# Kernel optimization log

Measured on AMD Instinct MI355X. Metric: run time of the kernel, lower is better.

Reference implementation:

```python
import jax, jax.numpy as jnp
import numpy as np

HIDDEN = 512
N_CLASSES = 10

def setup_inputs() -> dict:
    key = jax.random.key(0)
    ks = jax.random.split(key, 7)
    B, T, H = 256, 784, HIDDEN
    s_ih = 1.0 / np.sqrt(H)
    inputs = jax.random.normal(ks[0], (B, T), dtype=jnp.float32)
    # nn.LSTMCell(1, H) parameters, gate order i, f, g, o
    W_ih = jax.random.uniform(ks[1], (4 * H, 1), jnp.float32, -s_ih, s_ih)
    W_hh = jax.random.uniform(ks[2], (4 * H, H), jnp.float32, -s_ih, s_ih)
    b_ih = jax.random.uniform(ks[3], (4 * H,), jnp.float32, -s_ih, s_ih)
    b_hh = jax.random.uniform(ks[4], (4 * H,), jnp.float32, -s_ih, s_ih)
    # nn.Linear(H, 10)
    W_lin = jax.random.uniform(ks[5], (N_CLASSES, H), jnp.float32, -s_ih, s_ih)
    b_lin = jax.random.uniform(ks[6], (N_CLASSES,), jnp.float32, -s_ih, s_ih)
    return {"inputs": inputs, "W_ih": W_ih, "W_hh": W_hh, "b_ih": b_ih,
            "b_hh": b_hh, "W_lin": W_lin, "b_lin": b_lin}

def reference(inputs, W_ih, W_hh, b_ih, b_hh, W_lin, b_lin):
    B = inputs.shape[0]
    H = W_hh.shape[1]
    w_in = W_ih[:, 0]          # [4H], input feature dim is 1
    bias = b_ih + b_hh         # [4H]

    def step(carry, x_t):
        h, c = carry
        # gates: [B, 4H] = x contribution + recurrent matmul + bias
        gates = x_t[:, None] * w_in[None, :] + h @ W_hh.T + bias
        i, f, g, o = jnp.split(gates, 4, axis=1)
        c_new = jax.nn.sigmoid(f) * c + jax.nn.sigmoid(i) * jnp.tanh(g)
        h_new = jax.nn.sigmoid(o) * jnp.tanh(c_new)
        return (h_new, c_new), None

    h0 = jnp.zeros((B, H), dtype=inputs.dtype)
    c0 = jnp.zeros((B, H), dtype=inputs.dtype)
    (h_T, _), _ = jax.lax.scan(step, (h0, c0), inputs.T)  # scan over T
    return h_T @ W_lin.T + b_lin  # [B, n_classes]
```

## Files before the change

kernel.cpp:

```cpp
#include <hip/hip_runtime.h>
#include <hip/hip_bf16.h>
#include <cmath>

#define HID 512
#define TSTEPS 784
#define BATCH 256
#define NCLS 10
#define NBLK 256
#define NGRP 16

typedef __bf16 bf16x8 __attribute__((ext_vector_type(8)));
typedef float f32x4 __attribute__((ext_vector_type(4)));
typedef float f32x2 __attribute__((ext_vector_type(2)));
typedef int   i32x4 __attribute__((ext_vector_type(4)));

#define SWS(r) (((unsigned)(r) & 7u) << 4)

#define LDX4_CC(dst, addr) \
    asm volatile("global_load_dwordx4 %0, %1, off sc0 sc1" : "=v"(dst) : "v"(addr) : "memory")
#define STOREDW_CC(addr, val) \
    asm volatile("global_store_dword %0, %1, off sc0 sc1" :: "v"(addr), "v"(val) : "memory")

__device__ __forceinline__ unsigned lddw_cc_wait(const unsigned* a) {
    unsigned d;
    asm volatile("global_load_dword %0, %1, off sc0 sc1\n\ts_waitcnt vmcnt(0)"
                 : "=v"(d) : "v"(a) : "memory");
    return d;
}

__global__ void init_all(const float* __restrict__ x, float* __restrict__ xT,
                         uint4* __restrict__ hz, unsigned* __restrict__ flg) {
    int t = blockIdx.x, tid = threadIdx.x;
    xT[t * BATCH + tid] = x[tid * TSTEPS + t];
    int i = t * 256 + tid;
    if (i < (512 << 10) / 16) hz[i] = make_uint4(0u, 0u, 0u, 0u);
    if (i < NGRP * 64) flg[i] = 0u;
}

__device__ __forceinline__ float sigmoid_f(float v) {
    return __fdividef(1.f, 1.f + __expf(-v));
}
__device__ __forceinline__ float tanh_f(float v) {
    float e = __expf(fminf(fmaxf(2.f * v, -30.f), 30.f));
    return __fdividef(e - 1.f, e + 1.f);
}

__global__ __launch_bounds__(512)
void lstm_persist(const float* __restrict__ xT,
                  const float* __restrict__ W_hh,
                  const float* __restrict__ w_in,
                  const float* __restrict__ b_ih,
                  const float* __restrict__ b_hh,
                  __bf16* __restrict__ h0,
                  __bf16* __restrict__ h1,
                  float* __restrict__ hf,
                  unsigned* __restrict__ flg)
{
    __shared__ __align__(16) __bf16 wlds[128 * HID];
    __shared__ __align__(16) __bf16 hlds[16 * HID];
    __shared__ float gl[4][16][33];
    __shared__ float xl[16];

    const int tid  = threadIdx.x;
    const int lane = tid & 63;
    const int w    = tid >> 6;
    const int s    = w & 3;
    const int ch   = w >> 2;
    const int bg   = blockIdx.x >> 4;
    const int cs   = blockIdx.x & 15;
    const int b0   = bg * 16;
    const int j0   = cs * 32;
    const int rlo  = lane & 15;
    const int khi  = (lane >> 4) * 8;

    unsigned* flags = flg + bg * 64;

    {
        int r = tid >> 2;
        int q = tid & 3;
        int gs = r >> 5, jj = r & 31;
        const float* src = W_hh + (size_t)(gs * HID + j0 + jj) * HID + q * 128;
        char* wp = (char*)wlds;
        unsigned rowb = (unsigned)r * (HID * 2);
        unsigned sw   = SWS(r);
        #pragma unroll
        for (int cc = 0; cc < 128; cc += 8) {
            float4 va = *(const float4*)(src + cc);
            float4 vb = *(const float4*)(src + cc + 4);
            bf16x8 pk;
            pk[0]=(__bf16)va.x; pk[1]=(__bf16)va.y; pk[2]=(__bf16)va.z; pk[3]=(__bf16)va.w;
            pk[4]=(__bf16)vb.x; pk[5]=(__bf16)vb.y; pk[6]=(__bf16)vb.z; pk[7]=(__bf16)vb.w;
            *(bf16x8*)(wp + ((rowb + (unsigned)(q * 128 + cc) * 2) ^ sw)) = pk;
        }
    }

    float win_l, bias_l;
    {
        int idx = s * HID + j0 + ch * 16 + rlo;
        win_l  = w_in[idx];
        bias_l = b_ih[idx] + b_hh[idx];
    }

    const int Rc  = tid >> 5;
    const int col = tid & 31;
    float creg = 0.f;

    const int rS  = tid >> 5;
    const int seg = tid & 31;
    const unsigned rowbS = (unsigned)rS * (HID * 2);
    const unsigned swS   = SWS(rS);
    const unsigned* myflag = flags + (seg >> 1);

    const unsigned rBb = (unsigned)(s * 32 + ch * 16 + rlo) * (HID * 2);
    const unsigned swB = SWS(rlo);
    const char* wbp = (const char*)wlds;
    const char* hbp = (const char*)hlds;
    char* hwp = (char*)hlds;

    __syncthreads();

    for (int t = 0; t < TSTEPS; ++t) {
        const __bf16* hprev = (t & 1) ? h1 : h0;
        __bf16* hnext       = (t & 1) ? h0 : h1;

        if (tid < 16) xl[tid] = xT[t * BATCH + b0 + tid];
        {
            while (lddw_cc_wait(myflag) < (unsigned)t) __builtin_amdgcn_s_sleep(1);
            const __bf16* gsrc = hprev + (size_t)(b0 + rS) * HID + seg * 16;
            i32x4 v0, v1;
            LDX4_CC(v0, gsrc);
            LDX4_CC(v1, gsrc + 8);
            asm volatile("s_waitcnt vmcnt(0)" ::: "memory");
            __builtin_amdgcn_sched_barrier(0);
            unsigned base = rowbS + (unsigned)seg * 32u;
            *(i32x4*)(hwp + ((base +  0u) ^ swS)) = v0;
            *(i32x4*)(hwp + ((base + 16u) ^ swS)) = v1;
        }
        __syncthreads();

        f32x4 acc_e, acc_o = {0.f,0.f,0.f,0.f};
        #pragma unroll
        for (int rr = 0; rr < 4; ++rr)
            acc_e[rr] = xl[(lane >> 4) * 4 + rr] * win_l + bias_l;
        #pragma unroll
        for (int ks = 0; ks < 16; ks += 2) {
            unsigned colb0 = (unsigned)(khi * 2 + ks * 64);
            unsigned colb1 = colb0 + 64u;
            bf16x8 a0 = *(const bf16x8*)(hbp + (((unsigned)rlo * 1024u + colb0) ^ SWS(rlo)));
            bf16x8 b0f = *(const bf16x8*)(wbp + ((rBb + colb0) ^ swB));
            bf16x8 a1 = *(const bf16x8*)(hbp + (((unsigned)rlo * 1024u + colb1) ^ SWS(rlo)));
            bf16x8 b1f = *(const bf16x8*)(wbp + ((rBb + colb1) ^ swB));
            acc_e = __builtin_amdgcn_mfma_f32_16x16x32_bf16(a0, b0f, acc_e, 0, 0, 0);
            acc_o = __builtin_amdgcn_mfma_f32_16x16x32_bf16(a1, b1f, acc_o, 0, 0, 0);
        }
        f32x4 acc0 = acc_e + acc_o;
        #pragma unroll
        for (int rr = 0; rr < 4; ++rr) {
            int rowl = (lane >> 4) * 4 + rr;
            gl[s][rowl][ch * 16 + rlo] = acc0[rr];
        }
        __syncthreads();

        {
            float gi = gl[0][Rc][col];
            float gf = gl[1][Rc][col];
            float gg = gl[2][Rc][col];
            float go = gl[3][Rc][col];
            float cn = sigmoid_f(gf) * creg + sigmoid_f(gi) * tanh_f(gg);
            creg = cn;
            float hn = sigmoid_f(go) * tanh_f(cn);
            float hn_o = __shfl_xor(hn, 1);
            if (t == TSTEPS - 1) {
                if (!(tid & 1))
                    *(f32x2*)(hf + (size_t)(b0 + Rc) * HID + j0 + col) = (f32x2){hn, hn_o};
            } else {
                if (!(tid & 1)) {
                    union { __bf16 b[2]; int i; } u;
                    u.b[0] = (__bf16)hn; u.b[1] = (__bf16)hn_o;
                    __bf16* dst = hnext + (size_t)(b0 + Rc) * HID + j0 + col;
                    STOREDW_CC(dst, u.i);
                }
            }
        }
        if (t == TSTEPS - 1) break;

        asm volatile("s_waitcnt vmcnt(0)" ::: "memory");
        __syncthreads();
        if (tid == 0) STOREDW_CC(flags + cs, (int)(t + 1));
    }
}

__global__ void head(const float* __restrict__ hfp, const float* __restrict__ Wl,
                     const float* __restrict__ bl_, float* __restrict__ out)
{
    __shared__ float hr[HID];
    int b = blockIdx.x;
    for (int k = threadIdx.x; k < HID; k += blockDim.x) hr[k] = hfp[b * HID + k];
    __syncthreads();
    int j = threadIdx.x;
    if (j < NCLS) {
        float acc = bl_[j];
        for (int k = 0; k < HID; ++k) acc += hr[k] * Wl[j * HID + k];
        out[b * NCLS + j] = acc;
    }
}

extern "C" void kernel_launch(void* const* d_in, const int* in_sizes, int n_in,
                              void* d_out, int out_size, void* d_ws, size_t ws_size,
                              hipStream_t stream) {
    const float* inputs = (const float*)d_in[0];
    const float* W_ih   = (const float*)d_in[1];
    const float* W_hh   = (const float*)d_in[2];
    const float* b_ih   = (const float*)d_in[3];
    const float* b_hh   = (const float*)d_in[4];
    const float* W_lin  = (const float*)d_in[5];
    const float* b_lin  = (const float*)d_in[6];

    const size_t OFS_H1  = 256u << 10;
    const size_t OFS_HF  = 512u << 10;
    const size_t OFS_XT  = 1024u << 10;
    const size_t OFS_FLG = OFS_XT + (size_t)TSTEPS * BATCH * 4;
    const size_t NEEDED  = OFS_FLG + NGRP * 64 * 4;
    if (ws_size < NEEDED) return;

    char* ws = (char*)d_ws;
    __bf16* h0 = (__bf16*)ws;
    __bf16* h1 = (__bf16*)(ws + OFS_H1);
    float*  hf = (float*)(ws + OFS_HF);
    float*  xT = (float*)(ws + OFS_XT);
    unsigned* flg = (unsigned*)(ws + OFS_FLG);

    init_all<<<TSTEPS, BATCH, 0, stream>>>(inputs, xT, (uint4*)h0, flg);

    lstm_persist<<<NBLK, 512, 0, stream>>>(xT, W_hh, W_ih, b_ih, b_hh,
                                           h0, h1, hf, flg);

    head<<<BATCH, 64, 0, stream>>>(hf, W_lin, b_lin, (float*)d_out);
}
```

Measured before the change: 2.698 ms.

## Interleave gate rows in LDS weights so each wave computes full LSTM cells via shuffles

Reorders the bf16 W_hh rows in shared memory so that the four gates (i,f,g,o) of each hidden unit sit in adjacent MFMA output columns within one wave. The cell update then runs on the MFMA accumulators directly using lane shuffles, which removes the gate staging array in LDS and one block-wide barrier per timestep. In exchange, every lane evaluates all four gate nonlinearities redundantly across the 4-lane group, and the h stores become narrower and more scattered.

```diff
diff --git a/kernel.cpp b/kernel.cpp
--- a/kernel.cpp
+++ b/kernel.cpp
@@ -58,14 +58,11 @@
 {
     __shared__ __align__(16) __bf16 wlds[128 * HID];
     __shared__ __align__(16) __bf16 hlds[16 * HID];
-    __shared__ float gl[4][16][33];
     __shared__ float xl[16];
 
     const int tid  = threadIdx.x;
     const int lane = tid & 63;
     const int w    = tid >> 6;
-    const int s    = w & 3;
-    const int ch   = w >> 2;
     const int bg   = blockIdx.x >> 4;
     const int cs   = blockIdx.x & 15;
     const int b0   = bg * 16;
@@ -78,8 +75,9 @@
     {
         int r = tid >> 2;
         int q = tid & 3;
-        int gs = r >> 5, jj = r & 31;
-        const float* src = W_hh + (size_t)(gs * HID + j0 + jj) * HID + q * 128;
+        int wv = r >> 4, tc = r & 15;
+        int g = tc & 3, jj = tc >> 2;
+        const float* src = W_hh + (size_t)(g * HID + j0 + wv * 4 + jj) * HID + q * 128;
         char* wp = (char*)wlds;
         unsigned rowb = (unsigned)r * (HID * 2);
         unsigned sw   = SWS(r);
@@ -94,16 +92,15 @@
         }
     }
 
+    const int g_l  = rlo & 3;
+    const int jj_l = rlo >> 2;
     float win_l, bias_l;
     {
-        int idx = s * HID + j0 + ch * 16 + rlo;
+        int idx = g_l * HID + j0 + w * 4 + jj_l;
         win_l  = w_in[idx];
         bias_l = b_ih[idx] + b_hh[idx];
     }
-
-    const int Rc  = tid >> 5;
-    const int col = tid & 31;
-    float creg = 0.f;
+    float creg4[4] = {0.f, 0.f, 0.f, 0.f};
 
     const int rS  = tid >> 5;
     const int seg = tid & 31;
@@ -111,7 +108,7 @@
     const unsigned swS   = SWS(rS);
     const unsigned* myflag = flags + (seg >> 1);
 
-    const unsigned rBb = (unsigned)(s * 32 + ch * 16 + rlo) * (HID * 2);
+    const unsigned rBb = (unsigned)(w * 16 + rlo) * (HID * 2);
     const unsigned swB = SWS(rlo);
     const char* wbp = (const char*)wlds;
     const char* hbp = (const char*)hlds;
@@ -153,32 +150,28 @@
             acc_e = __builtin_amdgcn_mfma_f32_16x16x32_bf16(a0, b0f, acc_e, 0, 0, 0);
             acc_o = __builtin_amdgcn_mfma_f32_16x16x32_bf16(a1, b1f, acc_o, 0, 0, 0);
         }
-        f32x4 acc0 = acc_e + acc_o;
-        #pragma unroll
-        for (int rr = 0; rr < 4; ++rr) {
-            int rowl = (lane >> 4) * 4 + rr;
-            gl[s][rowl][ch * 16 + rlo] = acc0[rr];
-        }
-        __syncthreads();
 
         {
-            float gi = gl[0][Rc][col];
-            float gf = gl[1][Rc][col];
-            float gg = gl[2][Rc][col];
-            float go = gl[3][Rc][col];
-            float cn = sigmoid_f(gf) * creg + sigmoid_f(gi) * tanh_f(gg);
-            creg = cn;
-            float hn = sigmoid_f(go) * tanh_f(cn);
-            float hn_o = __shfl_xor(hn, 1);
-            if (t == TSTEPS - 1) {
-                if (!(tid & 1))
-                    *(f32x2*)(hf + (size_t)(b0 + Rc) * HID + j0 + col) = (f32x2){hn, hn_o};
-            } else {
-                if (!(tid & 1)) {
-                    union { __bf16 b[2]; int i; } u;
-                    u.b[0] = (__bf16)hn; u.b[1] = (__bf16)hn_o;
-                    __bf16* dst = hnext + (size_t)(b0 + Rc) * HID + j0 + col;
-                    STOREDW_CC(dst, u.i);
+            #pragma unroll
+            for (int rr = 0; rr < 4; ++rr) {
+                float sum = acc_e[rr] + acc_o[rr];
+                float vf = __shfl_xor(sum, 1);
+                float vg = __shfl_xor(sum, 2);
+                float vo = __shfl_xor(sum, 3);
+                float cn = sigmoid_f(vf) * creg4[rr] + sigmoid_f(sum) * tanh_f(vg);
+                creg4[rr] = cn;
+                float hn = sigmoid_f(vo) * tanh_f(cn);
+                float hp = __shfl_xor(hn, 4);
+                if ((lane & 7) == 0) {
+                    int row = (lane >> 4) * 4 + rr;
+                    int colb = j0 + w * 4 + jj_l;
+                    if (t == TSTEPS - 1) {
+                        *(f32x2*)(hf + (size_t)(b0 + row) * HID + colb) = (f32x2){hn, hp};
+                    } else {
+                        union { __bf16 b[2]; int i; } u;
+                        u.b[0] = (__bf16)hn; u.b[1] = (__bf16)hp;
+                        STOREDW_CC(hnext + (size_t)(b0 + row) * HID + colb, u.i);
+                    }
                 }
             }
         }
```

New measurement: 3.511 ms. 1.3x slower.
